# Optimization experiments

Hardware: AMD Instinct MI355X
Metric: run time of the kernel (lower is better)

## Reference

```python
import jax, jax.numpy as jnp
import numpy as np

WS = 4        # window_size
SHIFT = 3     # shift_size
HEADS = 4
DIM = 128
HR, WR = 256, 256  # input_resolution (matches post-upsample H, W)


def _rel_pos_index(ws):
    coords = np.stack(np.meshgrid(np.arange(ws), np.arange(ws), indexing='ij'))  # (2, ws, ws)
    cf = coords.reshape(2, -1)
    rel = (cf[:, :, None] - cf[:, None, :]).transpose(1, 2, 0).astype(np.int64)
    rel[:, :, 0] += ws - 1
    rel[:, :, 1] += ws - 1
    rel[:, :, 0] *= 2 * ws - 1
    return rel.sum(-1)  # (N, N)


def _attn_mask(H, W, ws, shift):
    img = np.zeros((H, W))
    cnt = 0
    sl = (slice(0, -ws), slice(-ws, -shift), slice(-shift, None))
    for hs in sl:
        for wsl in sl:
            img[hs, wsl] = cnt
            cnt += 1
    mw = img.reshape(H // ws, ws, W // ws, ws).transpose(0, 2, 1, 3).reshape(-1, ws * ws)
    diff = mw[:, None, :] - mw[:, :, None]  # unsqueeze(1) - unsqueeze(2)
    return np.where(diff != 0, -100.0, 0.0).astype(np.float32)  # (nW, N, N)


REL_IDX = jnp.asarray(_rel_pos_index(WS))
ATTN_MASK = jnp.asarray(_attn_mask(HR, WR, WS, SHIFT))


def _upsample2x_ac(x):
    def interp(x, axis):
        n = x.shape[axis]
        m = 2 * n
        pos = jnp.arange(m) * ((n - 1) / (m - 1))
        lo = jnp.floor(pos).astype(jnp.int32)
        hi = jnp.minimum(lo + 1, n - 1)
        w = (pos - lo).astype(x.dtype)
        shp = [1] * x.ndim
        shp[axis] = m
        w = w.reshape(shp)
        return jnp.take(x, lo, axis=axis) * (1 - w) + jnp.take(x, hi, axis=axis) * w
    return interp(interp(x, 2), 3)


def _conv2d(x, w, b, pad):
    y = jax.lax.conv_general_dilated(x, w, (1, 1), [(pad, pad), (pad, pad)],
                                     dimension_numbers=('NCHW', 'OIHW', 'NCHW'))
    return y + b[None, :, None, None]


def _bn(x, g, b, m, v):
    # eval-mode BatchNorm2d
    s = g / jnp.sqrt(v + 1e-5)
    return x * s[None, :, None, None] + (b - m * s)[None, :, None, None]


def setup_inputs():
    key = jax.random.key(0)
    ks = jax.random.split(key, 8)
    f = jax.random.normal
    return {
        'x': f(ks[0], (4, 256, 128, 64), jnp.float32),
        'qkv_w': f(ks[1], (DIM, 3 * DIM), jnp.float32) * 0.02,
        'qkv_b': jnp.zeros((3 * DIM,), jnp.float32),
        'proj_w': f(ks[2], (DIM, DIM), jnp.float32) * 0.02,
        'proj_b': jnp.zeros((DIM,), jnp.float32),
        'rpb': f(ks[3], ((2 * WS - 1) ** 2, HEADS), jnp.float32) * 0.02,
        'conv1_w': f(ks[4], (256, 256, 3, 3), jnp.float32) * 0.02,
        'conv1_b': jnp.zeros((256,), jnp.float32),
        'bn1_g': jnp.ones((256,), jnp.float32),
        'bn1_b': jnp.zeros((256,), jnp.float32),
        'bn1_m': jnp.zeros((256,), jnp.float32),
        'bn1_v': jnp.ones((256,), jnp.float32),
        'conv2_w': f(ks[5], (256, 256, 3, 3), jnp.float32) * 0.02,
        'conv2_b': jnp.zeros((256,), jnp.float32),
        'bn2_g': jnp.ones((256,), jnp.float32),
        'bn2_b': jnp.zeros((256,), jnp.float32),
        'bn2_m': jnp.zeros((256,), jnp.float32),
        'bn2_v': jnp.ones((256,), jnp.float32),
        'idc_w': f(ks[6], (256, 256, 1, 1), jnp.float32) * 0.02,
        'idc_b': jnp.zeros((256,), jnp.float32),
        'bni_g': jnp.ones((256,), jnp.float32),
        'bni_b': jnp.zeros((256,), jnp.float32),
        'bni_m': jnp.zeros((256,), jnp.float32),
        'bni_v': jnp.ones((256,), jnp.float32),
    }


def reference(x, qkv_w, qkv_b, proj_w, proj_b, rpb,
              conv1_w, conv1_b, bn1_g, bn1_b, bn1_m, bn1_v,
              conv2_w, conv2_b, bn2_g, bn2_b, bn2_m, bn2_v,
              idc_w, idc_b, bni_g, bni_b, bni_m, bni_v):
    x = _upsample2x_ac(x)                 # (B, 256, 256, 128), treated as (B,H,W,C) downstream
    B, H, W, C = x.shape
    shortcut = x
    xs = jnp.roll(x, (-SHIFT, -SHIFT), axis=(1, 2))
    # window partition -> (B*nW, N, C)
    nWh, nWw = H // WS, W // WS
    xw = xs.reshape(B, nWh, WS, nWw, WS, C).transpose(0, 1, 3, 2, 4, 5).reshape(-1, WS * WS, C)
    B_, N, _ = xw.shape
    hd = C // HEADS
    qkv = (xw @ qkv_w + qkv_b).reshape(B_, N, 3, HEADS, hd).transpose(2, 0, 3, 1, 4)
    q, k, v = qkv[0], qkv[1], qkv[2]
    attn = jnp.einsum('bhnd,bhmd->bhnm', q * (hd ** -0.5), k)
    bias = rpb[REL_IDX.reshape(-1)].reshape(N, N, HEADS).transpose(2, 0, 1)  # (h, N, N)
    attn = attn + bias[None]
    nW = ATTN_MASK.shape[0]
    attn = attn.reshape(B_ // nW, nW, HEADS, N, N) + ATTN_MASK[None, :, None]
    attn = jax.nn.softmax(attn.reshape(B_, HEADS, N, N), axis=-1)
    out = jnp.einsum('bhnm,bhmd->bhnd', attn, v).transpose(0, 2, 1, 3).reshape(B_, N, C)
    out = out @ proj_w + proj_b
    # window reverse + roll back
    out = out.reshape(B, nWh, nWw, WS, WS, C).transpose(0, 1, 3, 2, 4, 5).reshape(B, H, W, C)
    out = jnp.roll(out, (SHIFT, SHIFT), axis=(1, 2))
    x = shortcut + out
    # DoubleConv with identity branch (tensor treated as NCHW, per original code)
    y = _conv2d(x, conv1_w, conv1_b, 1)
    y = jax.nn.relu(_bn(y, bn1_g, bn1_b, bn1_m, bn1_v))
    y = _conv2d(y, conv2_w, conv2_b, 1)
    y = _bn(y, bn2_g, bn2_b, bn2_m, bn2_v)
    idn = _bn(_conv2d(x, idc_w, idc_b, 0), bni_g, bni_b, bni_m, bni_v)
    return jax.nn.relu(y + idn)
```

## Files before the change

### kernel.cpp

```cpp
#include <hip/hip_runtime.h>
#include <hip/hip_bf16.h>
#include <math.h>
#include <cstddef>

#define BATCH 4
#define WDIM 256
#define CDIM 128
#define WS 4
#define SHIFT 3
#define HEADS 4
#define HD 32
#define NTOK 16

typedef __attribute__((ext_vector_type(8))) short short8;
typedef __attribute__((ext_vector_type(4))) int int4v;
typedef __attribute__((ext_vector_type(4))) float f32x4;

__device__ __forceinline__ int regionOf(int v) {
    return v < (WDIM - WS) ? 0 : (v < (WDIM - SHIFT) ? 1 : 2);
}

__device__ __forceinline__ short f2bf(float v) {
    __hip_bfloat16 h = __float2bfloat16(v);
    return __builtin_bit_cast(short, h);
}
__device__ __forceinline__ float bf2f(short s) {
    unsigned u = ((unsigned)(unsigned short)s) << 16;
    return __builtin_bit_cast(float, u);
}

__global__ __launch_bounds__(256) void repack_attnw(
    const float* __restrict__ qkv_w,
    const float* __restrict__ proj_w,
    __hip_bfloat16* __restrict__ qkvw_rep,
    __hip_bfloat16* __restrict__ projw_rep)
{
    int idx = blockIdx.x * 256 + threadIdx.x;
    if (idx < 49152) {
        int j = idx >> 7, c = idx & 127;
        qkvw_rep[idx] = __float2bfloat16(qkv_w[c * 384 + j]);
    } else {
        int k = idx - 49152;
        int j = k >> 7, c = k & 127;
        projw_rep[k] = __float2bfloat16(proj_w[c * 128 + j]);
    }
}

#define XROW_RS 2114

__global__ __launch_bounds__(256, 4) void attn_kernel(
    const float* __restrict__ xin,
    const __hip_bfloat16* __restrict__ qkvw_rep,
    const __hip_bfloat16* __restrict__ projw_rep,
    const float* __restrict__ qkv_b,
    const float* __restrict__ proj_b,
    const float* __restrict__ rpb,
    __hip_bfloat16* __restrict__ xatt)
{
    __shared__ __align__(16) char smem[40864];
    float* xrowF  = (float*)smem;
    short* qkvs   = (short*)smem;
    short* aoutS  = (short*)smem;
    short* Xb     = (short*)(smem + 16912);
    short* Ps     = (short*)(smem + 25616);
    short* Vt     = (short*)(smem + 29712);
    float* rpbs   = (float*)(smem + 37904);
    float* qkvbS  = (float*)(smem + 38688);
    float* projbS = (float*)(smem + 40224);
    float* tokw2  = (float*)(smem + 40736);

    const int tid = threadIdx.x;
    const int bid = blockIdx.x;
    const int l   = tid & 63;
    const int wv  = tid >> 6;
    const int lm  = l & 15;
    const int lq  = l >> 4;

    if (tid < 196) rpbs[tid] = rpb[tid];
    for (int i = tid; i < 384; i += 256) qkvbS[i] = qkv_b[i];
    if (tid < 128) projbS[tid] = proj_b[tid];

    #pragma unroll
    for (int k = 0; k < 4; k++) {
        int id = tid + k * 256;
        int n   = id >> 5;
        int row = (id >> 4) & 1;
        int ll  = id & 15;
        int w_  = n >> 4, nn = n & 15;
        int win = bid * 2 + w_;
        int b   = win >> 12;
        int wh  = (win >> 6) & 63;
        int ww  = win & 63;
        int r = nn >> 2, c = nn & 3;
        int gh = (wh * 4 + r + SHIFT) & 255;
        int gw = (ww * 4 + c + SHIFT) & 255;
        float pos2 = gw * (127.0f / 255.0f);
        int lo2 = (int)floorf(pos2);
        int hi2 = min(lo2 + 1, 127);
        if (row == 0 && ll == 0) tokw2[n] = pos2 - (float)lo2;
        int src = row == 0 ? lo2 : hi2;
        const float4* rp = (const float4*)(xin + (((size_t)b * 256 + gh) * 128 + src) * 64);
        float4 v = rp[ll];
        float* bp = xrowF + row * XROW_RS + n + (4 * ll) * 33;
        bp[0]      = v.x;
        bp[33]     = v.y;
        bp[66]     = v.z;
        bp[99]     = v.w;
    }
    __syncthreads();

    {
        int n = tid >> 3;
        int jj = tid & 7;
        float w2 = tokw2[n];
        const float* x0 = xrowF + n;
        const float* x1 = x0 + XROW_RS;
        #pragma unroll
        for (int p = 0; p < 8; p++) {
            unsigned pk = 0;
            #pragma unroll
            for (int q = 0; q < 2; q++) {
                int cc = jj * 16 + p * 2 + q;
                float pos3 = cc * (63.0f / 127.0f);
                int lo3 = (int)floorf(pos3);
                float w3 = pos3 - (float)lo3;
                int o = lo3 * 33;
                float v0 = x0[o] * (1.f - w3) + x0[o + 33] * w3;
                float v1 = x1[o] * (1.f - w3) + x1[o + 33] * w3;
                float out = v0 * (1.f - w2) + v1 * w2;
                pk |= ((unsigned)(unsigned short)f2bf(out)) << (16 * q);
            }
            *(unsigned*)&Xb[n * 136 + jj * 16 + p * 2] = pk;
        }
    }
    __syncthreads();

    {
        f32x4 qacc[6][2];
        #pragma unroll
        for (int a = 0; a < 6; a++)
            #pragma unroll
            for (int t = 0; t < 2; t++) qacc[a][t] = (f32x4)0.0f;

        for (int ks = 0; ks < 4; ks++) {
            short8 af[6];
            #pragma unroll
            for (int jj = 0; jj < 6; jj++) {
                const int4v* gp = (const int4v*)(qkvw_rep +
                    (size_t)(wv * 96 + jj * 16 + lm) * 128 + ks * 32 + lq * 8);
                af[jj] = __builtin_bit_cast(short8, *gp);
            }
            short8 bfr[2];
            #pragma unroll
            for (int tt = 0; tt < 2; tt++)
                bfr[tt] = *(const short8*)&Xb[(tt * 16 + lm) * 136 + ks * 32 + lq * 8];
            #pragma unroll
            for (int jj = 0; jj < 6; jj++)
                #pragma unroll
                for (int tt = 0; tt < 2; tt++)
                    qacc[jj][tt] = __builtin_amdgcn_mfma_f32_16x16x32_bf16(
                        af[jj], bfr[tt], qacc[jj][tt], 0, 0, 0);
        }
        #pragma unroll
        for (int jj = 0; jj < 6; jj++) {
            int jbase = wv * 96 + jj * 16 + lq * 4;
            #pragma unroll
            for (int tt = 0; tt < 2; tt++) {
                int tok = tt * 16 + lm;
                if (jbase < 128) {
                    float v0 = (qacc[jj][tt][0] + qkvbS[jbase+0]) * 0.17677669529663687f;
                    float v1 = (qacc[jj][tt][1] + qkvbS[jbase+1]) * 0.17677669529663687f;
                    float v2 = (qacc[jj][tt][2] + qkvbS[jbase+2]) * 0.17677669529663687f;
                    float v3 = (qacc[jj][tt][3] + qkvbS[jbase+3]) * 0.17677669529663687f;
                    unsigned p0 = (unsigned short)f2bf(v0) | ((unsigned)(unsigned short)f2bf(v1) << 16);
                    unsigned p1 = (unsigned short)f2bf(v2) | ((unsigned)(unsigned short)f2bf(v3) << 16);
                    *(unsigned*)&qkvs[tok * 264 + jbase]     = p0;
                    *(unsigned*)&qkvs[tok * 264 + jbase + 2] = p1;
                } else if (jbase < 256) {
                    float v0 = qacc[jj][tt][0] + qkvbS[jbase+0];
                    float v1 = qacc[jj][tt][1] + qkvbS[jbase+1];
                    float v2 = qacc[jj][tt][2] + qkvbS[jbase+2];
                    float v3 = qacc[jj][tt][3] + qkvbS[jbase+3];
                    unsigned p0 = (unsigned short)f2bf(v0) | ((unsigned)(unsigned short)f2bf(v1) << 16);
                    unsigned p1 = (unsigned short)f2bf(v2) | ((unsigned)(unsigned short)f2bf(v3) << 16);
                    *(unsigned*)&qkvs[tok * 264 + jbase]     = p0;
                    *(unsigned*)&qkvs[tok * 264 + jbase + 2] = p1;
                } else {
                    #pragma unroll
                    for (int r = 0; r < 4; r++) {
                        int d = jbase - 256 + r;
                        Vt[(tt * 128 + d) * 16 + lm] = f2bf(qacc[jj][tt][r] + qkvbS[jbase + r]);
                    }
                }
            }
        }
    }
    __syncthreads();

    {
        int w_ = wv >> 1;
        int hb = (wv & 1) * 2;
        int win = bid * 2 + w_;
        int wh = (win >> 6) & 63;
        int ww = win & 63;
        int nq = lm;
        int r1 = nq >> 2, c1 = nq & 3;
        int reg1 = regionOf(wh * 4 + r1) * 3 + regionOf(ww * 4 + c1);
        #pragma unroll
        for (int hh = 0; hh < 2; hh++) {
            int h = hb + hh;
            short8 qa = *(const short8*)&qkvs[(w_ * 16 + lm) * 264 + h * 32 + lq * 8];
            short8 kb = *(const short8*)&qkvs[(w_ * 16 + lm) * 264 + 128 + h * 32 + lq * 8];
            f32x4 s = __builtin_amdgcn_mfma_f32_16x16x32_bf16(kb, qa, (f32x4)0.0f, 0, 0, 0);
            float v[4];
            #pragma unroll
            for (int r = 0; r < 4; r++) {
                int m = lq * 4 + r;
                int r2 = m >> 2, c2 = m & 3;
                int ridx = (r1 - r2 + 3) * 7 + (c1 - c2 + 3);
                v[r] = s[r] + rpbs[ridx * 4 + h];
                int reg2 = regionOf(wh * 4 + r2) * 3 + regionOf(ww * 4 + c2);
                if (reg2 != reg1) v[r] -= 100.f;
            }
            float mx = fmaxf(fmaxf(v[0], v[1]), fmaxf(v[2], v[3]));
            mx = fmaxf(mx, __shfl_xor(mx, 16));
            mx = fmaxf(mx, __shfl_xor(mx, 32));
            float e0 = __expf(v[0] - mx);
            float e1 = __expf(v[1] - mx);
            float e2 = __expf(v[2] - mx);
            float e3 = __expf(v[3] - mx);
            float ss = (e0 + e1) + (e2 + e3);
            ss += __shfl_xor(ss, 16);
            ss += __shfl_xor(ss, 32);
            float rinv = 1.0f / ss;
            unsigned plo = (unsigned short)f2bf(e0 * rinv) |
                           ((unsigned)(unsigned short)f2bf(e1 * rinv) << 16);
            unsigned phi = (unsigned short)f2bf(e2 * rinv) |
                           ((unsigned)(unsigned short)f2bf(e3 * rinv) << 16);
            unsigned long long pk = (unsigned long long)plo |
                                    ((unsigned long long)phi << 32);
            *(unsigned long long*)&Ps[((w_ * 4 + h) * 16 + lm) * 16 + lq * 4] = pk;
        }
    }
    __syncthreads();

    {
        int w_ = wv >> 1;
        int hb = (wv & 1) * 2;
        #pragma unroll
        for (int hh = 0; hh < 2; hh++) {
            int h = hb + hh;
            #pragma unroll
            for (int dt = 0; dt < 2; dt++) {
                short8 pa = (short8)0;
                short8 vb = (short8)0;
                if (lq < 2) {
                    pa = *(const short8*)&Ps[((w_ * 4 + h) * 16 + lm) * 16 + lq * 8];
                    vb = *(const short8*)&Vt[(w_ * 128 + h * 32 + dt * 16 + lm) * 16 + lq * 8];
                }
                f32x4 o = __builtin_amdgcn_mfma_f32_16x16x32_bf16(pa, vb, (f32x4)0.0f, 0, 0, 0);
                #pragma unroll
                for (int r = 0; r < 4; r++) {
                    aoutS[(w_ * 16 + lq * 4 + r) * 136 + h * 32 + dt * 16 + lm] = f2bf(o[r]);
                }
            }
        }
    }
    __syncthreads();

    {
        f32x4 cacc[2][2];
        #pragma unroll
        for (int a = 0; a < 2; a++)
            #pragma unroll
            for (int t = 0; t < 2; t++) cacc[a][t] = (f32x4)0.0f;

        for (int ks = 0; ks < 4; ks++) {
            short8 af[2];
            #pragma unroll
            for (int jj = 0; jj < 2; jj++) {
                const int4v* gp = (const int4v*)(projw_rep +
                    (size_t)(wv * 32 + jj * 16 + lm) * 128 + ks * 32 + lq * 8);
                af[jj] = __builtin_bit_cast(short8, *gp);
            }
            short8 bfr[2];
            #pragma unroll
            for (int tt = 0; tt < 2; tt++)
                bfr[tt] = *(const short8*)&aoutS[(tt * 16 + lm) * 136 + ks * 32 + lq * 8];
            #pragma unroll
            for (int jj = 0; jj < 2; jj++)
                #pragma unroll
                for (int tt = 0; tt < 2; tt++)
                    cacc[jj][tt] = __builtin_amdgcn_mfma_f32_16x16x32_bf16(
                        af[jj], bfr[tt], cacc[jj][tt], 0, 0, 0);
        }
        __syncthreads();
        #pragma unroll
        for (int jj = 0; jj < 2; jj++) {
            int jbase = wv * 32 + jj * 16 + lq * 4;
            #pragma unroll
            for (int tt = 0; tt < 2; tt++) {
                int tok = tt * 16 + lm;
                float v0 = cacc[jj][tt][0] + projbS[jbase+0] + bf2f(Xb[tok * 136 + jbase+0]);
                float v1 = cacc[jj][tt][1] + projbS[jbase+1] + bf2f(Xb[tok * 136 + jbase+1]);
                float v2 = cacc[jj][tt][2] + projbS[jbase+2] + bf2f(Xb[tok * 136 + jbase+2]);
                float v3 = cacc[jj][tt][3] + projbS[jbase+3] + bf2f(Xb[tok * 136 + jbase+3]);
                unsigned p0 = (unsigned short)f2bf(v0) | ((unsigned)(unsigned short)f2bf(v1) << 16);
                unsigned p1 = (unsigned short)f2bf(v2) | ((unsigned)(unsigned short)f2bf(v3) << 16);
                *(unsigned*)&aoutS[tok * 136 + jbase]     = p0;
                *(unsigned*)&aoutS[tok * 136 + jbase + 2] = p1;
            }
        }
    }
    __syncthreads();

    {
        #pragma unroll
        for (int k = 0; k < 4; k++) {
            int idx = k * 256 + tid;
            int j  = idx & 127;
            int c  = (idx >> 7) & 3;
            int w_ = idx >> 9;
            int win = bid * 2 + w_;
            int b   = win >> 12;
            int wh  = (win >> 6) & 63;
            int ww  = win & 63;
            int gw  = (ww * 4 + c + SHIFT) & 255;
            int slot0 = (wh * 4 + SHIFT + 1) & 255;
            unsigned short s0 = (unsigned short)aoutS[(w_ * 16 + 0 + c) * 136 + j];
            unsigned short s1 = (unsigned short)aoutS[(w_ * 16 + 4 + c) * 136 + j];
            unsigned short s2 = (unsigned short)aoutS[(w_ * 16 + 8 + c) * 136 + j];
            unsigned short s3 = (unsigned short)aoutS[(w_ * 16 + 12 + c) * 136 + j];
            unsigned long long pk =
                (unsigned long long)s0 | ((unsigned long long)s1 << 16) |
                ((unsigned long long)s2 << 32) | ((unsigned long long)s3 << 48);
            size_t base = (((size_t)b * 256 + gw) * 128 + j) * 256 + slot0;
            *(unsigned long long*)(xatt + base) = pk;
        }
    }
}

__global__ __launch_bounds__(256) void repack3(
    const float* __restrict__ w, const float* __restrict__ bias,
    const float* __restrict__ g_, const float* __restrict__ b_,
    const float* __restrict__ m_, const float* __restrict__ v_,
    __hip_bfloat16* __restrict__ wrep, float* __restrict__ cconst, int roll)
{
    int idx = blockIdx.x * 256 + threadIdx.x;
    int co = idx / 2304;
    int rem = idx - co * 2304;
    int ci = rem / 9;
    int tap = rem - ci * 9;
    float s = g_[co] * rsqrtf(v_[co] + 1e-5f);
    int ci_s = (ci + roll) & 255;
    size_t o = ((((size_t)(co >> 7) * 8 + (ci_s >> 5)) * 9 + tap) * 128 + (co & 127)) * 32 + (ci_s & 31);
    wrep[o] = __float2bfloat16(w[idx] * s);
    if (rem == 0) cconst[co] = bias[co] * s + (b_[co] - m_[co] * s);
}

__global__ __launch_bounds__(256) void repack1(
    const float* __restrict__ w, const float* __restrict__ bias,
    const float* __restrict__ g_, const float* __restrict__ b_,
    const float* __restrict__ m_, const float* __restrict__ v_,
    __hip_bfloat16* __restrict__ wrep, float* __restrict__ cconst)
{
    int idx = blockIdx.x * 256 + threadIdx.x;
    int co = idx >> 8, ci = idx & 255;
    float s = g_[co] * rsqrtf(v_[co] + 1e-5f);
    int ci_s = (ci + 1) & 255;
    wrep[(((size_t)(co >> 7) * 8 + (ci_s >> 5)) * 128 + (co & 127)) * 32 + (ci_s & 31)] =
        __float2bfloat16(w[idx] * s);
    if (ci == 0) cconst[co] += bias[co] * s + (b_[co] - m_[co] * s);
}

template<int HAS_IDC, int OUT_BF16>
__global__ __launch_bounds__(256) void conv_mfma(
    const __hip_bfloat16* __restrict__ xin,
    const __hip_bfloat16* __restrict__ xidc,
    const __hip_bfloat16* __restrict__ wrep,
    const __hip_bfloat16* __restrict__ wrepi,
    const float* __restrict__ cconst,
    void* __restrict__ outp)
{
    constexpr int NROWS = HAS_IDC ? 6 : 4;
    constexpr int NPER  = NROWS * 2;
    constexpr int NTAPS = HAS_IDC ? 10 : 9;
    __shared__ __align__(16) short xs[NROWS * 130 * 40];

    const int tid = threadIdx.x;
    const int l  = tid & 63;
    const int wv = tid >> 6;
    const int wave_co = (wv & 1) * 64;
    const int wave_w  = (wv >> 1) * 64;
    const int nb = ((blockIdx.x & 7) << 7) | (blockIdx.x >> 3);
    const int g  = nb & 1;
    const int hp = (nb >> 1) & 127;
    const int n  = nb >> 8;
    const int h0 = hp * 2;
    const int lq = l >> 4;
    const int lm = l & 15;

    {
        int row  = tid >> 6;
        int side = (tid >> 5) & 1;
        int ci   = tid & 31;
        xs[(row * 130 + (side ? 129 : 0)) * 40 + ci] = 0;
    }

    f32x4 acc[2][4][4];
    #pragma unroll
    for (int r = 0; r < 2; r++)
        #pragma unroll
        for (int a = 0; a < 4; a++)
            #pragma unroll
            for (int b = 0; b < 4; b++) acc[r][a][b] = (f32x4)0.0f;

    #pragma unroll 1
    for (int cb = 0; cb < 8; cb++) {
        __syncthreads();
        int4v tmp[NPER];
        #pragma unroll
        for (int t = 0; t < NPER; t++) {
            int idx = t * 256 + tid;
            int c8  = idx & 3;
            int w   = (idx >> 2) & 127;
            int row = idx >> 9;
            int4v v = {0, 0, 0, 0};
            if (!HAS_IDC || row < 4) {
                int hh = h0 - 1 + row;
                if (0 <= hh && hh < 256)
                    v = *(const int4v*)(xin + ((((size_t)n * 256 + hh) * 128 + w) << 8)
                                        + cb * 32 + c8 * 8);
            } else {
                int hh = h0 + (row - 4);
                v = *(const int4v*)(xidc + ((((size_t)n * 256 + hh) * 128 + w) << 8)
                                    + cb * 32 + c8 * 8);
            }
            tmp[t] = v;
        }
        #pragma unroll
        for (int t = 0; t < NPER; t++) {
            int idx = t * 256 + tid;
            int c8  = idx & 3;
            int w   = (idx >> 2) & 127;
            int row = idx >> 9;
            *(int4v*)&xs[(row * 130 + w + 1) * 40 + c8 * 8] = tmp[t];
        }
        __syncthreads();

        #pragma unroll 1
        for (int tap = 0; tap < NTAPS; tap++) {
            const __hip_bfloat16* ap = (!HAS_IDC || tap < 9)
                ? wrep + (((size_t)(g * 8 + cb) * 9 + tap) << 12)
                : wrepi + (((size_t)(g * 8 + cb)) << 12);
            short8 afr[4];
            #pragma unroll
            for (int cs = 0; cs < 4; cs++)
                afr[cs] = __builtin_bit_cast(short8,
                    *(const int4v*)(ap + (size_t)(wave_co + cs * 16 + lm) * 32 + lq * 8));
            #pragma unroll
            for (int r = 0; r < 2; r++) {
                const short* bs;
                if (HAS_IDC && tap == 9) {
                    bs = xs + ((4 + r) * 130 + wave_w + 1) * 40;
                } else {
                    int kh = tap / 3, kw = tap - kh * 3;
                    bs = xs + ((kh + r) * 130 + wave_w + kw) * 40;
                }
                #pragma unroll
                for (int ws = 0; ws < 4; ws++) {
                    short8 bfr = __builtin_bit_cast(short8,
                        *(const int4v*)&bs[(ws * 16 + lm) * 40 + lq * 8]);
                    #pragma unroll
                    for (int cs = 0; cs < 4; cs++)
                        acc[r][cs][ws] = __builtin_amdgcn_mfma_f32_16x16x32_bf16(
                            afr[cs], bfr, acc[r][cs][ws], 0, 0, 0);
                }
            }
        }
    }

    #pragma unroll
    for (int cs = 0; cs < 4; cs++) {
        int co0 = g * 128 + wave_co + cs * 16 + lq * 4;
        float c0 = cconst[co0 + 0], c1 = cconst[co0 + 1];
        float c2 = cconst[co0 + 2], c3 = cconst[co0 + 3];
        #pragma unroll
        for (int r = 0; r < 2; r++) {
            int h = h0 + r;
            #pragma unroll
            for (int ws = 0; ws < 4; ws++) {
                int w = wave_w + ws * 16 + lm;
                float v0 = fmaxf(acc[r][cs][ws][0] + c0, 0.f);
                float v1 = fmaxf(acc[r][cs][ws][1] + c1, 0.f);
                float v2 = fmaxf(acc[r][cs][ws][2] + c2, 0.f);
                float v3 = fmaxf(acc[r][cs][ws][3] + c3, 0.f);
                if (OUT_BF16) {
                    unsigned long long pk =
                        (unsigned long long)(unsigned short)f2bf(v0) |
                        ((unsigned long long)(unsigned short)f2bf(v1) << 16) |
                        ((unsigned long long)(unsigned short)f2bf(v2) << 32) |
                        ((unsigned long long)(unsigned short)f2bf(v3) << 48);
                    size_t base = ((((size_t)n * 256 + h) * 128 + w) << 8) + co0;
                    *(unsigned long long*)((__hip_bfloat16*)outp + base) = pk;
                } else {
                    float* op = (float*)outp;
                    op[(((size_t)n * 256 + co0 + 0) * 256 + h) * 128 + w] = v0;
                    op[(((size_t)n * 256 + co0 + 1) * 256 + h) * 128 + w] = v1;
                    op[(((size_t)n * 256 + co0 + 2) * 256 + h) * 128 + w] = v2;
                    op[(((size_t)n * 256 + co0 + 3) * 256 + h) * 128 + w] = v3;
                }
            }
        }
    }
}

extern "C" void kernel_launch(void* const* d_in, const int* in_sizes, int n_in,
                              void* d_out, int out_size, void* d_ws, size_t ws_size,
                              hipStream_t stream) {
    const float* x       = (const float*)d_in[0];
    const float* qkv_w   = (const float*)d_in[1];
    const float* qkv_b   = (const float*)d_in[2];
    const float* proj_w  = (const float*)d_in[3];
    const float* proj_b  = (const float*)d_in[4];
    const float* rpb     = (const float*)d_in[5];
    const float* conv1_w = (const float*)d_in[6];
    const float* conv1_b = (const float*)d_in[7];
    const float* bn1_g   = (const float*)d_in[8];
    const float* bn1_b   = (const float*)d_in[9];
    const float* bn1_m   = (const float*)d_in[10];
    const float* bn1_v   = (const float*)d_in[11];
    const float* conv2_w = (const float*)d_in[12];
    const float* conv2_b = (const float*)d_in[13];
    const float* bn2_g   = (const float*)d_in[14];
    const float* bn2_b   = (const float*)d_in[15];
    const float* bn2_m   = (const float*)d_in[16];
    const float* bn2_v   = (const float*)d_in[17];
    const float* idc_w   = (const float*)d_in[18];
    const float* idc_b   = (const float*)d_in[19];
    const float* bni_g   = (const float*)d_in[20];
    const float* bni_b   = (const float*)d_in[21];
    const float* bni_m   = (const float*)d_in[22];
    const float* bni_v   = (const float*)d_in[23];

    const size_t TE = (size_t)BATCH * 256 * 256 * 128;
    char* ws = (char*)d_ws;
    __hip_bfloat16* xatt  = (__hip_bfloat16*)(ws);
    __hip_bfloat16* y1    = (__hip_bfloat16*)(ws + TE * 2);
    __hip_bfloat16* wrep1 = (__hip_bfloat16*)(ws + TE * 4);
    __hip_bfloat16* wrep2 = (__hip_bfloat16*)(ws + TE * 4 + 1179648);
    __hip_bfloat16* wrepi = (__hip_bfloat16*)(ws + TE * 4 + 2359296);
    float*          c1    = (float*)(ws + TE * 4 + 2490368);
    float*          c2    = (float*)(ws + TE * 4 + 2491392);
    __hip_bfloat16* qkvw_rep = (__hip_bfloat16*)(ws + TE * 4 + 2492416);
    __hip_bfloat16* projw_rep= (__hip_bfloat16*)(ws + TE * 4 + 2590720);

    repack3<<<2304, 256, 0, stream>>>(conv1_w, conv1_b, bn1_g, bn1_b, bn1_m, bn1_v, wrep1, c1, 1);
    repack3<<<2304, 256, 0, stream>>>(conv2_w, conv2_b, bn2_g, bn2_b, bn2_m, bn2_v, wrep2, c2, 0);
    repack1<<<256, 256, 0, stream>>>(idc_w, idc_b, bni_g, bni_b, bni_m, bni_v, wrepi, c2);
    repack_attnw<<<256, 256, 0, stream>>>(qkv_w, proj_w, qkvw_rep, projw_rep);

    attn_kernel<<<8192, 256, 0, stream>>>(x, qkvw_rep, projw_rep, qkv_b, proj_b, rpb, xatt);

    conv_mfma<0, 1><<<1024, 256, 0, stream>>>(xatt, nullptr, wrep1, nullptr, c1, (void*)y1);
    conv_mfma<1, 0><<<1024, 256, 0, stream>>>(y1, xatt, wrep2, wrepi, c2, d_out);
}
```

Baseline: 831.4 us.

## Drop LDS staging in conv kernel, load MFMA operands directly from global

Rewrites the implicit-GEMM conv kernel to read B fragments straight from global memory (relying on cache) instead of staging input rows in shared memory with barriers. Each block now computes one output row instead of two, so the grid doubles. Zero padding is handled with clamped indices plus masks, and taps whose input row is out of bounds are skipped. This removes the LDS writes and syncs, at the cost of more redundant global/L2 traffic and the loss of row reuse across the two output rows.

```diff
diff --git a/kernel.cpp b/kernel.cpp
--- a/kernel.cpp
+++ b/kernel.cpp
@@ -382,100 +382,83 @@
     const float* __restrict__ cconst,
     void* __restrict__ outp)
 {
-    constexpr int NROWS = HAS_IDC ? 6 : 4;
-    constexpr int NPER  = NROWS * 2;
-    constexpr int NTAPS = HAS_IDC ? 10 : 9;
-    __shared__ __align__(16) short xs[NROWS * 130 * 40];
-
     const int tid = threadIdx.x;
     const int l  = tid & 63;
     const int wv = tid >> 6;
     const int wave_co = (wv & 1) * 64;
     const int wave_w  = (wv >> 1) * 64;
-    const int nb = ((blockIdx.x & 7) << 7) | (blockIdx.x >> 3);
-    const int g  = nb & 1;
-    const int hp = (nb >> 1) & 127;
-    const int n  = nb >> 8;
-    const int h0 = hp * 2;
+    const int nb = ((blockIdx.x & 7) << 8) | (blockIdx.x >> 3);
+    const int g = nb & 1;
+    const int h = (nb >> 1) & 255;
+    const int n = nb >> 9;
     const int lq = l >> 4;
     const int lm = l & 15;
 
-    {
-        int row  = tid >> 6;
-        int side = (tid >> 5) & 1;
-        int ci   = tid & 31;
-        xs[(row * 130 + (side ? 129 : 0)) * 40 + ci] = 0;
-    }
-
-    f32x4 acc[2][4][4];
+    f32x4 acc[4][4];
     #pragma unroll
-    for (int r = 0; r < 2; r++)
-        #pragma unroll
-        for (int a = 0; a < 4; a++)
-            #pragma unroll
-            for (int b = 0; b < 4; b++) acc[r][a][b] = (f32x4)0.0f;
+    for (int a = 0; a < 4; a++)
+        #pragma unroll
+        for (int b = 0; b < 4; b++) acc[a][b] = (f32x4)0.0f;
+
+    const __hip_bfloat16* rowp[3];
+    bool rowok[3];
+    #pragma unroll
+    for (int kh = 0; kh < 3; kh++) {
+        int hh = h - 1 + kh;
+        rowok[kh] = (0 <= hh && hh < 256);
+        int hcl = min(max(hh, 0), 255);
+        rowp[kh] = xin + (((size_t)(n * 256 + hcl) * 128) << 8);
+    }
+    const __hip_bfloat16* idcp = HAS_IDC
+        ? (xidc + (((size_t)(n * 256 + h) * 128) << 8)) : (const __hip_bfloat16*)nullptr;
 
     #pragma unroll 1
     for (int cb = 0; cb < 8; cb++) {
-        __syncthreads();
-        int4v tmp[NPER];
-        #pragma unroll
-        for (int t = 0; t < NPER; t++) {
-            int idx = t * 256 + tid;
-            int c8  = idx & 3;
-            int w   = (idx >> 2) & 127;
-            int row = idx >> 9;
-            int4v v = {0, 0, 0, 0};
-            if (!HAS_IDC || row < 4) {
-                int hh = h0 - 1 + row;
-                if (0 <= hh && hh < 256)
-                    v = *(const int4v*)(xin + ((((size_t)n * 256 + hh) * 128 + w) << 8)
-                                        + cb * 32 + c8 * 8);
-            } else {
-                int hh = h0 + (row - 4);
-                v = *(const int4v*)(xidc + ((((size_t)n * 256 + hh) * 128 + w) << 8)
-                                    + cb * 32 + c8 * 8);
-            }
-            tmp[t] = v;
-        }
-        #pragma unroll
-        for (int t = 0; t < NPER; t++) {
-            int idx = t * 256 + tid;
-            int c8  = idx & 3;
-            int w   = (idx >> 2) & 127;
-            int row = idx >> 9;
-            *(int4v*)&xs[(row * 130 + w + 1) * 40 + c8 * 8] = tmp[t];
-        }
-        __syncthreads();
-
-        #pragma unroll 1
-        for (int tap = 0; tap < NTAPS; tap++) {
-            const __hip_bfloat16* ap = (!HAS_IDC || tap < 9)
-                ? wrep + (((size_t)(g * 8 + cb) * 9 + tap) << 12)
-                : wrepi + (((size_t)(g * 8 + cb)) << 12);
+        #pragma unroll
+        for (int tap = 0; tap < 9; tap++) {
+            const int kh = tap / 3;
+            const int kw = tap - kh * 3;
+            if (!rowok[kh]) continue;
+            const __hip_bfloat16* ap = wrep + (((size_t)(g * 8 + cb) * 9 + tap) << 12);
             short8 afr[4];
             #pragma unroll
             for (int cs = 0; cs < 4; cs++)
                 afr[cs] = __builtin_bit_cast(short8,
                     *(const int4v*)(ap + (size_t)(wave_co + cs * 16 + lm) * 32 + lq * 8));
-            #pragma unroll
-            for (int r = 0; r < 2; r++) {
-                const short* bs;
-                if (HAS_IDC && tap == 9) {
-                    bs = xs + ((4 + r) * 130 + wave_w + 1) * 40;
-                } else {
-                    int kh = tap / 3, kw = tap - kh * 3;
-                    bs = xs + ((kh + r) * 130 + wave_w + kw) * 40;
+            const __hip_bfloat16* bp = rowp[kh] + cb * 32;
+            #pragma unroll
+            for (int ws = 0; ws < 4; ws++) {
+                int we = wave_w + ws * 16 + lm + kw - 1;
+                int wc = (kw == 0) ? max(we, 0) : ((kw == 2) ? min(we, 127) : we);
+                int4v bv = *(const int4v*)(bp + wc * 256 + lq * 8);
+                if (kw != 1) {
+                    int m = (we == wc) ? -1 : 0;
+                    int4v mv = {m, m, m, m};
+                    bv &= mv;
                 }
+                short8 bfr = __builtin_bit_cast(short8, bv);
                 #pragma unroll
-                for (int ws = 0; ws < 4; ws++) {
-                    short8 bfr = __builtin_bit_cast(short8,
-                        *(const int4v*)&bs[(ws * 16 + lm) * 40 + lq * 8]);
-                    #pragma unroll
-                    for (int cs = 0; cs < 4; cs++)
-                        acc[r][cs][ws] = __builtin_amdgcn_mfma_f32_16x16x32_bf16(
-                            afr[cs], bfr, acc[r][cs][ws], 0, 0, 0);
-                }
+                for (int cs = 0; cs < 4; cs++)
+                    acc[cs][ws] = __builtin_amdgcn_mfma_f32_16x16x32_bf16(
+                        afr[cs], bfr, acc[cs][ws], 0, 0, 0);
+            }
+        }
+        if constexpr (HAS_IDC) {
+            const __hip_bfloat16* ap = wrepi + (((size_t)(g * 8 + cb)) << 12);
+            short8 afr[4];
+            #pragma unroll
+            for (int cs = 0; cs < 4; cs++)
+                afr[cs] = __builtin_bit_cast(short8,
+                    *(const int4v*)(ap + (size_t)(wave_co + cs * 16 + lm) * 32 + lq * 8));
+            const __hip_bfloat16* bp = idcp + cb * 32;
+            #pragma unroll
+            for (int ws = 0; ws < 4; ws++) {
+                short8 bfr = __builtin_bit_cast(short8,
+                    *(const int4v*)(bp + (size_t)(wave_w + ws * 16 + lm) * 256 + lq * 8));
+                #pragma unroll
+                for (int cs = 0; cs < 4; cs++)
+                    acc[cs][ws] = __builtin_amdgcn_mfma_f32_16x16x32_bf16(
+                        afr[cs], bfr, acc[cs][ws], 0, 0, 0);
             }
         }
     }
@@ -486,30 +469,26 @@
         float c0 = cconst[co0 + 0], c1 = cconst[co0 + 1];
         float c2 = cconst[co0 + 2], c3 = cconst[co0 + 3];
         #pragma unroll
-        for (int r = 0; r < 2; r++) {
-            int h = h0 + r;
-            #pragma unroll
-            for (int ws = 0; ws < 4; ws++) {
-                int w = wave_w + ws * 16 + lm;
-                float v0 = fmaxf(acc[r][cs][ws][0] + c0, 0.f);
-                float v1 = fmaxf(acc[r][cs][ws][1] + c1, 0.f);
-                float v2 = fmaxf(acc[r][cs][ws][2] + c2, 0.f);
-                float v3 = fmaxf(acc[r][cs][ws][3] + c3, 0.f);
-                if (OUT_BF16) {
-                    unsigned long long pk =
-                        (unsigned long long)(unsigned short)f2bf(v0) |
-                        ((unsigned long long)(unsigned short)f2bf(v1) << 16) |
-                        ((unsigned long long)(unsigned short)f2bf(v2) << 32) |
-                        ((unsigned long long)(unsigned short)f2bf(v3) << 48);
-                    size_t base = ((((size_t)n * 256 + h) * 128 + w) << 8) + co0;
-                    *(unsigned long long*)((__hip_bfloat16*)outp + base) = pk;
-                } else {
-                    float* op = (float*)outp;
-                    op[(((size_t)n * 256 + co0 + 0) * 256 + h) * 128 + w] = v0;
-                    op[(((size_t)n * 256 + co0 + 1) * 256 + h) * 128 + w] = v1;
-                    op[(((size_t)n * 256 + co0 + 2) * 256 + h) * 128 + w] = v2;
-                    op[(((size_t)n * 256 + co0 + 3) * 256 + h) * 128 + w] = v3;
-                }
+        for (int ws = 0; ws < 4; ws++) {
+            int w = wave_w + ws * 16 + lm;
+            float v0 = fmaxf(acc[cs][ws][0] + c0, 0.f);
+            float v1 = fmaxf(acc[cs][ws][1] + c1, 0.f);
+            float v2 = fmaxf(acc[cs][ws][2] + c2, 0.f);
+            float v3 = fmaxf(acc[cs][ws][3] + c3, 0.f);
+            if (OUT_BF16) {
+                unsigned long long pk =
+                    (unsigned long long)(unsigned short)f2bf(v0) |
+                    ((unsigned long long)(unsigned short)f2bf(v1) << 16) |
+                    ((unsigned long long)(unsigned short)f2bf(v2) << 32) |
+                    ((unsigned long long)(unsigned short)f2bf(v3) << 48);
+                size_t base = ((((size_t)n * 256 + h) * 128 + w) << 8) + co0;
+                *(unsigned long long*)((__hip_bfloat16*)outp + base) = pk;
+            } else {
+                float* op = (float*)outp;
+                op[(((size_t)n * 256 + co0 + 0) * 256 + h) * 128 + w] = v0;
+                op[(((size_t)n * 256 + co0 + 1) * 256 + h) * 128 + w] = v1;
+                op[(((size_t)n * 256 + co0 + 2) * 256 + h) * 128 + w] = v2;
+                op[(((size_t)n * 256 + co0 + 3) * 256 + h) * 128 + w] = v3;
             }
         }
     }
@@ -562,6 +541,6 @@
 
     attn_kernel<<<8192, 256, 0, stream>>>(x, qkvw_rep, projw_rep, qkv_b, proj_b, rpb, xatt);
 
-    conv_mfma<0, 1><<<1024, 256, 0, stream>>>(xatt, nullptr, wrep1, nullptr, c1, (void*)y1);
-    conv_mfma<1, 0><<<1024, 256, 0, stream>>>(y1, xatt, wrep2, wrepi, c2, d_out);
-}
+    conv_mfma<0, 1><<<2048, 256, 0, stream>>>(xatt, nullptr, wrep1, nullptr, c1, (void*)y1);
+    conv_mfma<1, 0><<<2048, 256, 0, stream>>>(y1, xatt, wrep2, wrepi, c2, d_out);
+}
```

Measured after the change: 1.209 ms. 1.45x slower.
